# Performance work log

Measured on AMD Instinct MI355X. Metric: run time of the kernel, lower is better.

Reference implementation:

```python
import jax, jax.numpy as jnp
from jax import lax
import numpy as np

K = 3          # kernel size
KK = K * K
PAD = 1
STRIDE = 1
DIL = 1


def _bilinear_gather(img, ys, xs):
    # img: [B,C,H,W]; ys/xs: [B,KK,Ho,Wo] float sample coords.
    # torchvision deform_conv2d bilinear: zero outside, corner-wise validity.
    B, C, H, W = img.shape
    y0f = jnp.floor(ys)
    x0f = jnp.floor(xs)
    ly = ys - y0f
    lx = xs - x0f
    y0 = y0f.astype(jnp.int32)
    x0 = x0f.astype(jnp.int32)

    def corner(yi, xi):
        valid = (yi >= 0) & (yi < H) & (xi >= 0) & (xi < W)
        yc = jnp.clip(yi, 0, H - 1)
        xc = jnp.clip(xi, 0, W - 1)
        g = jax.vmap(lambda im, y, x: im[:, y, x])(img, yc, xc)  # [B,C,KK,Ho,Wo]
        return g * valid[:, None].astype(img.dtype)

    w00 = ((1 - ly) * (1 - lx))[:, None]
    w01 = ((1 - ly) * lx)[:, None]
    w10 = (ly * (1 - lx))[:, None]
    w11 = (ly * lx)[:, None]
    out = corner(y0, x0) * w00
    out = out + corner(y0, x0 + 1) * w01
    out = out + corner(y0 + 1, x0) * w10
    out = out + corner(y0 + 1, x0 + 1) * w11
    return out  # [B,C,KK,Ho,Wo]


def _deform_conv_forward(x, weight, bias, pg_w, pg_b):
    B, C, H, W = x.shape
    O = weight.shape[0]
    # offset/mask generator: 3x3 conv, stride 1, pad 1 -> [B, 3*KK, H, W]
    params = lax.conv_general_dilated(
        x, pg_w, window_strides=(1, 1), padding=[(1, 1), (1, 1)],
        dimension_numbers=('NCHW', 'OIHW', 'NCHW'))
    params = params + pg_b[None, :, None, None]
    oh, ow, m = jnp.split(params, 3, axis=1)          # each [B,KK,H,W]
    offset = jnp.concatenate([oh, ow], axis=1)        # [B,2*KK,H,W] (as in module)
    mask = jax.nn.sigmoid(m)                          # [B,KK,H,W]

    Ho = (H + 2 * PAD - DIL * (K - 1) - 1) // STRIDE + 1
    Wo = (W + 2 * PAD - DIL * (K - 1) - 1) // STRIDE + 1

    # torchvision layout: channel 2n = dy, 2n+1 = dx for kernel slot n
    off = offset.reshape(B, KK, 2, Ho, Wo)
    dy = off[:, :, 0]  # [B,KK,Ho,Wo]
    dx = off[:, :, 1]

    n = jnp.arange(KK)
    ki = (n // K).astype(x.dtype)   # kernel row offset
    kj = (n % K).astype(x.dtype)    # kernel col offset
    oy = (jnp.arange(Ho, dtype=x.dtype) * STRIDE - PAD)
    ox = (jnp.arange(Wo, dtype=x.dtype) * STRIDE - PAD)
    ys = oy[None, None, :, None] + (DIL * ki)[None, :, None, None] + dy
    xs = ox[None, None, None, :] + (DIL * kj)[None, :, None, None] + dx

    sampled = _bilinear_gather(x, ys, xs)             # [B,C,KK,Ho,Wo]
    sampled = sampled * mask[:, None]                 # modulated (DCNv2)

    w = weight.reshape(O, C, KK)
    out = jnp.einsum('bckhw,ock->bohw', sampled, w)
    out = out + bias[None, :, None, None]
    return out


def setup_inputs() -> dict:
    key = jax.random.key(0)
    k1, k2, k3, k4 = jax.random.split(key, 4)
    B, C, H, W, O = 4, 64, 128, 128, 64
    x = jax.random.normal(k1, (B, C, H, W), dtype=jnp.float32)
    weight = jax.random.normal(k2, (O, C, K, K), dtype=jnp.float32) * 0.05
    bias = jax.random.normal(k3, (O,), dtype=jnp.float32) * 0.05
    pg_w = jax.random.normal(k4, (3 * KK, C, 3, 3), dtype=jnp.float32) * 0.01
    pg_b = jnp.zeros((3 * KK,), dtype=jnp.float32)
    return {'x': x, 'weight': weight, 'bias': bias, 'pg_w': pg_w, 'pg_b': pg_b}


def reference(x, weight, bias, pg_w, pg_b):
    return _deform_conv_forward(x, weight, bias, pg_w, pg_b)
```

## Files before the change

kernel.cpp:

```cpp
#include <hip/hip_runtime.h>
#include <hip/hip_fp16.h>
#include <math.h>


typedef __attribute__((ext_vector_type(8))) short short8;
typedef __attribute__((ext_vector_type(8))) _Float16 f16x8;
typedef __attribute__((ext_vector_type(4))) float f32x4;

#define PSTR 2088

__device__ __forceinline__ unsigned short f2h(float f) {
    union { __half h; unsigned short s; } v; v.h = __float2half_rn(f); return v.s;
}
__device__ __forceinline__ f16x8 s2f(short8 s) {
    union { short8 s; f16x8 f; } u; u.s = s; return u.f;
}
__device__ __forceinline__ __half2 u2h2(unsigned u) {
    union { unsigned u; __half2 h; } v; v.u = u; return v.h;
}
__device__ __forceinline__ unsigned h22u(__half2 h) {
    union { __half2 h; unsigned u; } v; v.h = h; return v.u;
}
__device__ __forceinline__ unsigned uget(const uint4& v, int p) {
    return p == 0 ? v.x : p == 1 ? v.y : p == 2 ? v.z : v.w;
}

__global__ __launch_bounds__(256) void k_prep(const float* __restrict__ x,
                                              unsigned short* __restrict__ xh,
                                              const float* __restrict__ weight,
                                              const float* __restrict__ pg_w,
                                              unsigned short* __restrict__ wtF,
                                              unsigned short* __restrict__ pgwF) {
    __shared__ float tile[64][33];
    int bid = blockIdx.x;
    int t = threadIdx.x;
    if (bid < 2048) {
        int b = bid >> 9, h = (bid >> 2) & 127, w0 = (bid & 3) * 32;
        for (int idx = t; idx < 2048; idx += 256) {
            int c = idx >> 5, w = idx & 31;
            tile[c][w] = x[((b * 64 + c) * 128 + h) * 128 + w0 + w];
        }
        __syncthreads();
        {
            int wl = t >> 3, c0 = (t & 7) * 8;
            short8 v;
#pragma unroll
            for (int e = 0; e < 8; ++e) v[e] = (short)f2h(tile[c0 + e][wl]);
            *(short8*)&xh[(((size_t)b * 128 + h) * 128 + w0 + wl) * 64 + c0] = v;
        }
    } else {
        int idx = (bid - 2048) * 256 + t;
        if (idx < 36864) {
            int e = idx & 7, l = (idx >> 3) & 63, grp = idx >> 9;
            int nt = grp & 3, kb = (grp >> 2) & 1, kk = grp >> 3;
            int ln = l & 15, quad = l >> 4;
            int o = nt * 16 + ln;
            int c = kb * 32 + quad * 8 + e;
            wtF[idx] = f2h(weight[(o * 64 + c) * 9 + kk]);
        }
        int i2 = idx - 36864;
        if (i2 >= 0 && i2 < 18432) {
            int e = i2 & 7, l = (i2 >> 3) & 63, grp = i2 >> 9;
            int tl = grp & 1, kb = grp >> 1;
            int ln = l & 15, quad = l >> 4;
            int p = tl * 16 + ln;
            int k = kb * 32 + quad * 8 + e;
            float v = 0.f;
            if (p < 27) {
                int q = k >> 6, c = k & 63;
                v = pg_w[(p * 64 + c) * 9 + q];
            }
            pgwF[i2] = f2h(v);
        }
    }
}

__global__ __launch_bounds__(512) void k_fused(const unsigned short* __restrict__ xh,
                                               const unsigned short* __restrict__ pgwF,
                                               const float* __restrict__ pg_b,
                                               const unsigned short* __restrict__ wtF,
                                               const float* __restrict__ bias,
                                               float* __restrict__ out) {
    __shared__ unsigned short patch[8 * PSTR];
    __shared__ float P_s[27 * 129];

    int bid = blockIdx.x;
    int b  = bid >> 7;
    int h0 = ((bid >> 3) & 15) * 8;
    int w0 = (bid & 7) * 16;
    int t = threadIdx.x;
    int base_y = h0 - 2, base_x = w0 - 2;
    const unsigned short* xbb = xh + (size_t)b * 16384 * 64;

    for (int i = t; i < 2080; i += 512) {
        int yy = i / 160;
        int r  = i - yy * 160;
        int xx = r >> 3;
        int cg = r & 7;
        int gy = base_y + yy, gx = base_x + xx;
        int pos = yy * 20 + xx;
        short8 v = (short8)0;
        if (((unsigned)gy < 128u) && ((unsigned)gx < 128u))
            v = *(const short8*)&xbb[(gy * 128 + gx) * 64 + cg * 8];
        *(short8*)&patch[cg * PSTR + pos * 8] = v;
    }
    __syncthreads();

    int l = t & 63, w = t >> 6;
    int quad = l >> 4, ln = l & 15;
    int px = w * 16 + ln;
    int hh = h0 + w, ww = w0 + ln;

    {
        f32x4 o0 = {0.f, 0.f, 0.f, 0.f}, o1 = {0.f, 0.f, 0.f, 0.f};
#pragma unroll
        for (int kb = 0; kb < 18; ++kb) {
            int q = kb >> 1;
            int kh = q / 3, kw = q - 3 * (q / 3);
            short8 b0 = *(const short8*)&pgwF[(kb * 2 + 0) * 512 + l * 8];
            short8 b1 = *(const short8*)&pgwF[(kb * 2 + 1) * 512 + l * 8];
            int aoff = (w + kh + 1) * 20 + (ln + kw + 1);
            int cg = (kb & 1) * 4 + quad;
            short8 af = *(const short8*)&patch[cg * PSTR + aoff * 8];
            o0 = __builtin_amdgcn_mfma_f32_16x16x32_f16(s2f(af), s2f(b0), o0, 0, 0, 0);
            o1 = __builtin_amdgcn_mfma_f32_16x16x32_f16(s2f(af), s2f(b1), o1, 0, 0, 0);
        }
#pragma unroll
        for (int tile = 0; tile < 2; ++tile) {
            int p = tile * 16 + ln;
            f32x4 a = tile ? o1 : o0;
            if (p < 27) {
                float bo = pg_b[p];
#pragma unroll
                for (int i = 0; i < 4; ++i) {
                    int wpx = w * 16 + quad * 4 + i;
                    float v = a[i] + bo;
                    if (p >= 18) v = 1.f / (1.f + expf(-v));
                    P_s[p * 129 + wpx] = v;
                }
            }
        }
    }
    __syncthreads();

    f32x4 acc[4];
#pragma unroll
    for (int nt = 0; nt < 4; ++nt) acc[nt] = (f32x4){0.f, 0.f, 0.f, 0.f};

    int qbase = quad * PSTR;

    for (int kk = 0; kk < 9; ++kk) {
        short8 bfr[2][4];
#pragma unroll
        for (int kb = 0; kb < 2; ++kb)
#pragma unroll
            for (int nt = 0; nt < 4; ++nt)
                bfr[kb][nt] = *(const short8*)&wtF[((kk * 2 + kb) * 4 + nt) * 512 + l * 8];

        int ki = kk / 3, kj = kk - 3 * (kk / 3);
        float dyv = P_s[(2 * kk) * 129 + px];
        float dxv = P_s[(2 * kk + 1) * 129 + px];
        float m   = P_s[(18 + kk) * 129 + px];
        float ys = (float)(hh - 1 + ki) + dyv;
        float xs = (float)(ww - 1 + kj) + dxv;
        float y0f = floorf(ys), x0f = floorf(xs);
        int y0 = (int)y0f, x0 = (int)x0f;
        float ly = ys - y0f, lx = xs - x0f;
        float v0y = ((unsigned)y0 < 128u) ? 1.f : 0.f;
        float v1y = ((unsigned)(y0 + 1) < 128u) ? 1.f : 0.f;
        float v0x = ((unsigned)x0 < 128u) ? 1.f : 0.f;
        float v1x = ((unsigned)(x0 + 1) < 128u) ? 1.f : 0.f;
        float w00 = (1.f - ly) * (1.f - lx) * v0y * v0x * m;
        float w01 = (1.f - ly) * lx * v0y * v1x * m;
        float w10 = ly * (1.f - lx) * v1y * v0x * m;
        float w11 = ly * lx * v1y * v1x * m;
        int ly0 = y0 - base_y, lx0 = x0 - base_x;
        bool inp = ((unsigned)ly0 < 12u) && ((unsigned)lx0 < 18u);

        uint4 r[2][4];
        if (inp) {
            int pb = qbase + (ly0 * 20 + lx0) * 8;
#pragma unroll
            for (int kb = 0; kb < 2; ++kb) {
                int base = pb + kb * 4 * PSTR;
                r[kb][0] = *(const uint4*)&patch[base];
                r[kb][1] = *(const uint4*)&patch[base + 8];
                r[kb][2] = *(const uint4*)&patch[base + 160];
                r[kb][3] = *(const uint4*)&patch[base + 168];
            }
        } else {
            int y0c = min(max(y0, 0), 127), y1c = min(max(y0 + 1, 0), 127);
            int x0c = min(max(x0, 0), 127), x1c = min(max(x0 + 1, 0), 127);
            int base00 = (y0c * 128 + x0c) * 64;
            int dxo = (x1c - x0c) * 64, dyo = (y1c - y0c) * 8192;
#pragma unroll
            for (int kb = 0; kb < 2; ++kb) {
                int c0 = kb * 32 + quad * 8;
                r[kb][0] = *(const uint4*)&xbb[base00 + c0];
                r[kb][1] = *(const uint4*)&xbb[base00 + dxo + c0];
                r[kb][2] = *(const uint4*)&xbb[base00 + dyo + c0];
                r[kb][3] = *(const uint4*)&xbb[base00 + dyo + dxo + c0];
            }
        }

        __half2 W00 = __float2half2_rn(w00), W01 = __float2half2_rn(w01);
        __half2 W10 = __float2half2_rn(w10), W11 = __float2half2_rn(w11);
        f16x8 af[2];
#pragma unroll
        for (int kb = 0; kb < 2; ++kb) {
            union { unsigned u[4]; f16x8 f; } afu;
#pragma unroll
            for (int p = 0; p < 4; ++p) {
                __half2 v = __hmul2(W00, u2h2(uget(r[kb][0], p)));
                v = __hfma2(W01, u2h2(uget(r[kb][1], p)), v);
                v = __hfma2(W10, u2h2(uget(r[kb][2], p)), v);
                v = __hfma2(W11, u2h2(uget(r[kb][3], p)), v);
                afu.u[p] = h22u(v);
            }
            af[kb] = afu.f;
        }

#pragma unroll
        for (int kb = 0; kb < 2; ++kb)
#pragma unroll
            for (int nt = 0; nt < 4; ++nt)
                acc[nt] = __builtin_amdgcn_mfma_f32_16x16x32_f16(af[kb], s2f(bfr[kb][nt]), acc[nt], 0, 0, 0);
    }

    int ehh = h0 + w, eww = w0 + quad * 4;
#pragma unroll
    for (int nt = 0; nt < 4; ++nt) {
        int o = nt * 16 + ln;
        float bo = bias[o];
        float4 v;
        v.x = acc[nt][0] + bo; v.y = acc[nt][1] + bo;
        v.z = acc[nt][2] + bo; v.w = acc[nt][3] + bo;
        *(float4*)&out[((size_t)b * 64 + o) * 16384 + ehh * 128 + eww] = v;
    }
}

extern "C" void kernel_launch(void* const* d_in, const int* in_sizes, int n_in,
                              void* d_out, int out_size, void* d_ws, size_t ws_size,
                              hipStream_t stream) {
    const float* x      = (const float*)d_in[0];
    const float* weight = (const float*)d_in[1];
    const float* bias   = (const float*)d_in[2];
    const float* pg_w   = (const float*)d_in[3];
    const float* pg_b   = (const float*)d_in[4];
    float* out = (float*)d_out;

    unsigned short* xhB  = (unsigned short*)d_ws;
    unsigned short* wtF  = xhB + (size_t)4 * 16384 * 64;
    unsigned short* pgwF = wtF + 36864;

    k_prep<<<2264, 256, 0, stream>>>(x, xhB, weight, pg_w, wtF, pgwF);
    k_fused<<<512, 512, 0, stream>>>(xhB, pgwF, pg_b, wtF, bias, out);
}
```

Before: 97.57 us.

## Split channel reduction across two thread groups with shared-memory reduce

Doubles the block to 1024 threads and splits the K-dimension (channel halves) of both the offset-generator conv and the main deformable conv between two 512-thread groups. Each group gathers and interpolates only its half of the channels, then partial accumulators are summed through shared memory before the bias and output write. This is meant to expose more parallelism and latency hiding for the gather-heavy loop. In exchange it adds extra shared memory (a 16KB reduction buffer), two more barriers, and register pressure from the 1024-thread launch bound.

```diff
diff --git a/kernel.cpp b/kernel.cpp
--- a/kernel.cpp
+++ b/kernel.cpp
@@ -17,9 +17,6 @@
 }
 __device__ __forceinline__ __half2 u2h2(unsigned u) {
     union { unsigned u; __half2 h; } v; v.u = u; return v.h;
-}
-__device__ __forceinline__ unsigned h22u(__half2 h) {
-    union { __half2 h; unsigned u; } v; v.h = h; return v.u;
 }
 __device__ __forceinline__ unsigned uget(const uint4& v, int p) {
     return p == 0 ? v.x : p == 1 ? v.y : p == 2 ? v.z : v.w;
@@ -75,68 +72,81 @@
     }
 }
 
-__global__ __launch_bounds__(512) void k_fused(const unsigned short* __restrict__ xh,
-                                               const unsigned short* __restrict__ pgwF,
-                                               const float* __restrict__ pg_b,
-                                               const unsigned short* __restrict__ wtF,
-                                               const float* __restrict__ bias,
-                                               float* __restrict__ out) {
+__global__ __launch_bounds__(1024, 8) void k_fused(const unsigned short* __restrict__ xh,
+                                                   const unsigned short* __restrict__ pgwF,
+                                                   const float* __restrict__ pg_b,
+                                                   const unsigned short* __restrict__ wtF,
+                                                   const float* __restrict__ bias,
+                                                   float* __restrict__ out) {
     __shared__ unsigned short patch[8 * PSTR];
     __shared__ float P_s[27 * 129];
+    __shared__ f32x4 redv[1024];
 
     int bid = blockIdx.x;
     int b  = bid >> 7;
     int h0 = ((bid >> 3) & 15) * 8;
     int w0 = (bid & 7) * 16;
     int t = threadIdx.x;
+    int g  = t >> 9;
+    int tt = t & 511;
     int base_y = h0 - 2, base_x = w0 - 2;
     const unsigned short* xbb = xh + (size_t)b * 16384 * 64;
 
-    for (int i = t; i < 2080; i += 512) {
+    for (int i = t; i < 2080; i += 1024) {
         int yy = i / 160;
         int r  = i - yy * 160;
         int xx = r >> 3;
-        int cg = r & 7;
+        int cgr = r & 7;
         int gy = base_y + yy, gx = base_x + xx;
         int pos = yy * 20 + xx;
         short8 v = (short8)0;
         if (((unsigned)gy < 128u) && ((unsigned)gx < 128u))
-            v = *(const short8*)&xbb[(gy * 128 + gx) * 64 + cg * 8];
-        *(short8*)&patch[cg * PSTR + pos * 8] = v;
-    }
-    __syncthreads();
-
-    int l = t & 63, w = t >> 6;
+            v = *(const short8*)&xbb[(gy * 128 + gx) * 64 + cgr * 8];
+        *(short8*)&patch[cgr * PSTR + pos * 8] = v;
+    }
+    __syncthreads();
+
+    int l = tt & 63, wv = tt >> 6;
     int quad = l >> 4, ln = l & 15;
-    int px = w * 16 + ln;
-    int hh = h0 + w, ww = w0 + ln;
+    int px = wv * 16 + ln;
+    int hh = h0 + wv, ww = w0 + ln;
 
     {
         f32x4 o0 = {0.f, 0.f, 0.f, 0.f}, o1 = {0.f, 0.f, 0.f, 0.f};
 #pragma unroll
-        for (int kb = 0; kb < 18; ++kb) {
+        for (int j = 0; j < 9; ++j) {
+            int kb = g * 9 + j;
             int q = kb >> 1;
             int kh = q / 3, kw = q - 3 * (q / 3);
             short8 b0 = *(const short8*)&pgwF[(kb * 2 + 0) * 512 + l * 8];
             short8 b1 = *(const short8*)&pgwF[(kb * 2 + 1) * 512 + l * 8];
-            int aoff = (w + kh + 1) * 20 + (ln + kw + 1);
+            int aoff = (wv + kh + 1) * 20 + (ln + kw + 1);
             int cg = (kb & 1) * 4 + quad;
             short8 af = *(const short8*)&patch[cg * PSTR + aoff * 8];
             o0 = __builtin_amdgcn_mfma_f32_16x16x32_f16(s2f(af), s2f(b0), o0, 0, 0, 0);
             o1 = __builtin_amdgcn_mfma_f32_16x16x32_f16(s2f(af), s2f(b1), o1, 0, 0, 0);
         }
-#pragma unroll
-        for (int tile = 0; tile < 2; ++tile) {
-            int p = tile * 16 + ln;
-            f32x4 a = tile ? o1 : o0;
-            if (p < 27) {
-                float bo = pg_b[p];
-#pragma unroll
-                for (int i = 0; i < 4; ++i) {
-                    int wpx = w * 16 + quad * 4 + i;
-                    float v = a[i] + bo;
-                    if (p >= 18) v = 1.f / (1.f + expf(-v));
-                    P_s[p * 129 + wpx] = v;
+        if (g == 1) {
+            redv[tt * 2 + 0] = o0;
+            redv[tt * 2 + 1] = o1;
+        }
+        __syncthreads();
+        if (g == 0) {
+            o0 = o0 + redv[tt * 2 + 0];
+            o1 = o1 + redv[tt * 2 + 1];
+#pragma unroll
+            for (int tile = 0; tile < 2; ++tile) {
+                int p = tile * 16 + ln;
+                f32x4 a = tile ? o1 : o0;
+                if (p < 27) {
+                    float bo = pg_b[p];
+#pragma unroll
+                    for (int i = 0; i < 4; ++i) {
+                        int wpx = wv * 16 + quad * 4 + i;
+                        float v = a[i] + bo;
+                        if (p >= 18) v = 1.f / (1.f + expf(-v));
+                        P_s[p * 129 + wpx] = v;
+                    }
                 }
             }
         }
@@ -147,15 +157,13 @@
 #pragma unroll
     for (int nt = 0; nt < 4; ++nt) acc[nt] = (f32x4){0.f, 0.f, 0.f, 0.f};
 
-    int qbase = quad * PSTR;
+    int qbase = quad * PSTR + g * 4 * PSTR;
 
     for (int kk = 0; kk < 9; ++kk) {
-        short8 bfr[2][4];
-#pragma unroll
-        for (int kb = 0; kb < 2; ++kb)
-#pragma unroll
-            for (int nt = 0; nt < 4; ++nt)
-                bfr[kb][nt] = *(const short8*)&wtF[((kk * 2 + kb) * 4 + nt) * 512 + l * 8];
+        short8 bfr[4];
+#pragma unroll
+        for (int nt = 0; nt < 4; ++nt)
+            bfr[nt] = *(const short8*)&wtF[((kk * 2 + g) * 4 + nt) * 512 + l * 8];
 
         int ki = kk / 3, kj = kk - 3 * (kk / 3);
         float dyv = P_s[(2 * kk) * 129 + px];
@@ -177,65 +185,61 @@
         int ly0 = y0 - base_y, lx0 = x0 - base_x;
         bool inp = ((unsigned)ly0 < 12u) && ((unsigned)lx0 < 18u);
 
-        uint4 r[2][4];
+        uint4 r0, r1, r2, r3;
         if (inp) {
-            int pb = qbase + (ly0 * 20 + lx0) * 8;
-#pragma unroll
-            for (int kb = 0; kb < 2; ++kb) {
-                int base = pb + kb * 4 * PSTR;
-                r[kb][0] = *(const uint4*)&patch[base];
-                r[kb][1] = *(const uint4*)&patch[base + 8];
-                r[kb][2] = *(const uint4*)&patch[base + 160];
-                r[kb][3] = *(const uint4*)&patch[base + 168];
-            }
+            int base = qbase + (ly0 * 20 + lx0) * 8;
+            r0 = *(const uint4*)&patch[base];
+            r1 = *(const uint4*)&patch[base + 8];
+            r2 = *(const uint4*)&patch[base + 160];
+            r3 = *(const uint4*)&patch[base + 168];
         } else {
             int y0c = min(max(y0, 0), 127), y1c = min(max(y0 + 1, 0), 127);
             int x0c = min(max(x0, 0), 127), x1c = min(max(x0 + 1, 0), 127);
             int base00 = (y0c * 128 + x0c) * 64;
             int dxo = (x1c - x0c) * 64, dyo = (y1c - y0c) * 8192;
-#pragma unroll
-            for (int kb = 0; kb < 2; ++kb) {
-                int c0 = kb * 32 + quad * 8;
-                r[kb][0] = *(const uint4*)&xbb[base00 + c0];
-                r[kb][1] = *(const uint4*)&xbb[base00 + dxo + c0];
-                r[kb][2] = *(const uint4*)&xbb[base00 + dyo + c0];
-                r[kb][3] = *(const uint4*)&xbb[base00 + dyo + dxo + c0];
-            }
+            int c0 = g * 32 + quad * 8;
+            r0 = *(const uint4*)&xbb[base00 + c0];
+            r1 = *(const uint4*)&xbb[base00 + dxo + c0];
+            r2 = *(const uint4*)&xbb[base00 + dyo + c0];
+            r3 = *(const uint4*)&xbb[base00 + dyo + dxo + c0];
         }
 
         __half2 W00 = __float2half2_rn(w00), W01 = __float2half2_rn(w01);
         __half2 W10 = __float2half2_rn(w10), W11 = __float2half2_rn(w11);
-        f16x8 af[2];
-#pragma unroll
-        for (int kb = 0; kb < 2; ++kb) {
-            union { unsigned u[4]; f16x8 f; } afu;
-#pragma unroll
-            for (int p = 0; p < 4; ++p) {
-                __half2 v = __hmul2(W00, u2h2(uget(r[kb][0], p)));
-                v = __hfma2(W01, u2h2(uget(r[kb][1], p)), v);
-                v = __hfma2(W10, u2h2(uget(r[kb][2], p)), v);
-                v = __hfma2(W11, u2h2(uget(r[kb][3], p)), v);
-                afu.u[p] = h22u(v);
-            }
-            af[kb] = afu.f;
-        }
-
-#pragma unroll
-        for (int kb = 0; kb < 2; ++kb)
-#pragma unroll
-            for (int nt = 0; nt < 4; ++nt)
-                acc[nt] = __builtin_amdgcn_mfma_f32_16x16x32_f16(af[kb], s2f(bfr[kb][nt]), acc[nt], 0, 0, 0);
-    }
-
-    int ehh = h0 + w, eww = w0 + quad * 4;
-#pragma unroll
-    for (int nt = 0; nt < 4; ++nt) {
-        int o = nt * 16 + ln;
-        float bo = bias[o];
-        float4 v;
-        v.x = acc[nt][0] + bo; v.y = acc[nt][1] + bo;
-        v.z = acc[nt][2] + bo; v.w = acc[nt][3] + bo;
-        *(float4*)&out[((size_t)b * 64 + o) * 16384 + ehh * 128 + eww] = v;
+        union { unsigned u[4]; f16x8 f; } afu;
+#pragma unroll
+        for (int p = 0; p < 4; ++p) {
+            __half2 v = __hmul2(W00, u2h2(uget(r0, p)));
+            v = __hfma2(W01, u2h2(uget(r1, p)), v);
+            v = __hfma2(W10, u2h2(uget(r2, p)), v);
+            v = __hfma2(W11, u2h2(uget(r3, p)), v);
+            afu.u[p] = *(unsigned*)&v;
+        }
+
+#pragma unroll
+        for (int nt = 0; nt < 4; ++nt)
+            acc[nt] = __builtin_amdgcn_mfma_f32_16x16x32_f16(afu.f, s2f(bfr[nt]), acc[nt], 0, 0, 0);
+    }
+
+    __syncthreads();
+    f32x4* red2 = (f32x4*)patch;
+    if (g == 1) {
+#pragma unroll
+        for (int nt = 0; nt < 4; ++nt) red2[tt * 4 + nt] = acc[nt];
+    }
+    __syncthreads();
+    if (g == 0) {
+        int ehh = h0 + wv, eww = w0 + quad * 4;
+#pragma unroll
+        for (int nt = 0; nt < 4; ++nt) {
+            f32x4 s = acc[nt] + red2[tt * 4 + nt];
+            int o = nt * 16 + ln;
+            float bo = bias[o];
+            float4 v;
+            v.x = s[0] + bo; v.y = s[1] + bo;
+            v.z = s[2] + bo; v.w = s[3] + bo;
+            *(float4*)&out[((size_t)b * 64 + o) * 16384 + ehh * 128 + eww] = v;
+        }
     }
 }
 
@@ -254,5 +258,5 @@
     unsigned short* pgwF = wtF + 36864;
 
     k_prep<<<2264, 256, 0, stream>>>(x, xhB, weight, pg_w, wtF, pgwF);
-    k_fused<<<512, 512, 0, stream>>>(xhB, pgwF, pg_b, wtF, bias, out);
-}
+    k_fused<<<512, 1024, 0, stream>>>(xhB, pgwF, pg_b, wtF, bias, out);
+}
```

Measured after the change: 109.7 us. 12.5% more time.
